# Kernel tuning notes

Measured on AMD Instinct MI355X. Metric: run time of the kernel, lower is better.

## Reference

```python
import jax, jax.numpy as jnp
import numpy as np

B, S, H, Q = 32, 128, 128, 3  # users, seq_len, hidden_size, quadkey_level
L = Q - 1  # number of mixing scales


def setup_inputs() -> dict:
    key = jax.random.key(0)
    ks = jax.random.split(key, 12)
    trend0 = jax.random.normal(ks[0], (B, S, H), dtype=jnp.float32)
    trend1 = jax.random.normal(ks[1], (B, S, H), dtype=jnp.float32)
    trend2 = jax.random.normal(ks[2], (B, S, H), dtype=jnp.float32)
    # Per-position prefix linears padded into dense tensors, zero-masked beyond
    # the prefix length j+1 so the ragged math is exact:
    #   W1[j, :j+1, :j+1] ~ Linear(j+1, j+1), b1[j, :j+1]
    #   W2[j, :j+1]      ~ Linear(j+1, 1),   b2[j]
    idx = jnp.arange(S)
    pm = (idx[None, :] <= idx[:, None]).astype(jnp.float32)  # [j, s]: s <= j
    W1 = jax.random.normal(ks[3], (L, S, S, S), dtype=jnp.float32) * 0.05
    W1 = W1 * pm[None, :, :, None] * pm[None, :, None, :]
    b1 = jax.random.normal(ks[4], (L, S, S), dtype=jnp.float32) * 0.05 * pm[None]
    W2 = jax.random.normal(ks[5], (L, S, S), dtype=jnp.float32) * 0.05 * pm[None]
    b2 = jax.random.normal(ks[6], (L, S), dtype=jnp.float32) * 0.05
    # shared output MLP: Linear(H,H)->GELU->Linear(H,H); stored as [in, out]
    Wm1 = jax.random.normal(ks[7], (H, H), dtype=jnp.float32) * 0.05
    bm1 = jax.random.normal(ks[8], (H,), dtype=jnp.float32) * 0.05
    Wm2 = jax.random.normal(ks[9], (H, H), dtype=jnp.float32) * 0.05
    bm2 = jax.random.normal(ks[10], (H,), dtype=jnp.float32) * 0.05
    return {"trend0": trend0, "trend1": trend1, "trend2": trend2,
            "W1": W1, "b1": b1, "W2": W2, "b2": b2,
            "Wm1": Wm1, "bm1": bm1, "Wm2": Wm2, "bm2": bm2}


def reference(trend0, trend1, trend2, W1, b1, W2, b2, Wm1, bm1, Wm2, bm2):
    gelu = lambda x: jax.nn.gelu(x, approximate=False)  # torch nn.GELU default
    mlp = lambda x: gelu(x @ Wm1 + bm1) @ Wm2 + bm2

    rev = [trend2, trend1, trend0]  # trend_list reversed
    out_low = rev[0]
    out_high = rev[1]
    outs = [out_low]
    for i in range(Q - 1):
        # vectorized ragged prefix mix: per position j, out_low[:, :j+1] (as [B,H,j+1])
        # -> Linear(j+1,j+1) -> GELU -> Linear(j+1,1). Zero-padding in W1/b1/W2
        # kills all contributions beyond the prefix (GELU(0)=0).
        y1 = jnp.einsum('bsh,jst->bhjt', out_low, W1[i]) + b1[i]  # [B,H,S,S]
        res = jnp.einsum('bhjt,jt->bjh', gelu(y1), W2[i]) + b2[i][None, :, None]
        out_high = out_high + res
        out_low = out_high
        if i + 2 <= Q - 1:
            out_high = rev[i + 2]
        out_low = mlp(out_low)
        outs.append(out_low)
    outs.reverse()
    return tuple(outs)
```

## Files before the change

kernel.cpp:

```cpp
#include <hip/hip_runtime.h>
#include <stdint.h>

#define BSH (32 * 128 * 128)

typedef __attribute__((ext_vector_type(8))) __bf16 bf16x8;
typedef __attribute__((ext_vector_type(4))) float f32x4;

__device__ __forceinline__ unsigned short f2bf(float f) {
  union { float f; unsigned u; } v; v.f = f;
  return (unsigned short)((v.u + 0x7FFFu + ((v.u >> 16) & 1u)) >> 16);
}

__device__ __forceinline__ float fast_exp2(float x) {
#if __has_builtin(__builtin_amdgcn_exp2f)
  return __builtin_amdgcn_exp2f(x);
#else
  float r; asm("v_exp_f32 %0, %1" : "=v"(r) : "v"(x)); return r;
#endif
}
__device__ __forceinline__ float fast_rcp(float x) {
#if __has_builtin(__builtin_amdgcn_rcpf)
  return __builtin_amdgcn_rcpf(x);
#else
  float r; asm("v_rcp_f32 %0, %1" : "=v"(r) : "v"(x)); return r;
#endif
}

__device__ __forceinline__ float gelu_f(float y) {
  float u = y * y;
  float p = __builtin_fmaf(u, 0.044715f, 1.0f) * y;
  float w = fast_exp2(p * 2.30220787f);
  return y - y * fast_rcp(1.0f + w);
}

__device__ __forceinline__ void transpose_part(const float* __restrict__ src,
                                               unsigned short* __restrict__ dst,
                                               unsigned short* lds, int part) {
  const int tid = threadIdx.x;
  const float4* s4 = (const float4*)(src) + part * 1024;
  __syncthreads();
#pragma unroll
  for (int it = 0; it < 4; ++it) {
    int i4 = tid + it * 256;
    float4 v = s4[i4];
    int s = i4 >> 5;
    int t0 = (i4 * 4) & 127;
    unsigned short t[4] __attribute__((aligned(8)));
    t[0] = f2bf(v.x); t[1] = f2bf(v.y); t[2] = f2bf(v.z); t[3] = f2bf(v.w);
    *(uint2*)(lds + s * 136 + t0) = *(const uint2*)t;
  }
  __syncthreads();
#pragma unroll
  for (int it = 0; it < 2; ++it) {
    int c = tid + it * 256;
    int kql = c >> 7, tr = c & 127;
    unsigned short tmp[8] __attribute__((aligned(16)));
#pragma unroll
    for (int e = 0; e < 8; ++e) tmp[e] = lds[(kql * 8 + e) * 136 + tr];
    *(uint4*)(dst + ((part * 4 + kql) * 128 + tr) * 8) = *(const uint4*)tmp;
  }
}

__global__ __launch_bounds__(256) void prepass_kernel(
    const float* __restrict__ W1, const float* __restrict__ trend2,
    const float* __restrict__ Wm1, const float* __restrict__ Wm2,
    unsigned short* __restrict__ W1Tc, unsigned short* __restrict__ T2c,
    unsigned short* __restrict__ Wm1c, unsigned short* __restrict__ Wm2c,
    float* __restrict__ out2) {
  __shared__ __align__(16) unsigned short lds[32 * 136];
  const int bid = blockIdx.x;
  if (bid < 1024) {
    int part = bid >> 8, w = bid & 255;
    int x = w & 7, i = w >> 3;
    int stage = i >> 4, u = i & 15;
    int m = u & 7, half = u >> 3;
    int jpp = x + 8 * m;
    int j = half ? 127 - jpp : jpp;
    int blk = stage * 128 + j;
    transpose_part(W1 + blk * 16384, W1Tc + blk * 16384, lds, part);
  } else if (bid < 1152) {
    int t = bid - 1024;
    int part = t >> 5, b = t & 31;
    transpose_part(trend2 + b * 16384, T2c + b * 16384, lds, part);
    const float4* s4 = (const float4*)(trend2 + b * 16384);
    float4* d4 = (float4*)(out2 + b * 16384);
#pragma unroll
    for (int it = 0; it < 4; ++it) {
      int i = part * 1024 + threadIdx.x + it * 256;
      d4[i] = s4[i];
    }
  } else if (bid == 1152) {
#pragma unroll
    for (int part = 0; part < 4; ++part)
      transpose_part(Wm1, Wm1c, lds, part);
  } else {
#pragma unroll
    for (int part = 0; part < 4; ++part)
      transpose_part(Wm2, Wm2c, lds, part);
  }
}

__global__ __launch_bounds__(256, 3) void mix_mlp_kernel(
    const unsigned short* __restrict__ XTc,
    const unsigned short* __restrict__ W1Tj,
    const float* __restrict__ b1j,
    const float* __restrict__ W2j,
    const float* __restrict__ b2j,
    const float* __restrict__ trendR,
    const unsigned short* __restrict__ Wm1c,
    const unsigned short* __restrict__ Wm2c,
    const float* __restrict__ bm1,
    const float* __restrict__ bm2,
    float* __restrict__ outA,
    unsigned short* __restrict__ outTc) {
  __shared__ float res[512];
  __shared__ __align__(16) float xrow[2][128];
  __shared__ __align__(16) unsigned short urow[2][128];
  const int bid = blockIdx.x;
  const int b = bid >> 6;
  const int jp = bid & 63;
  const int js = jp, jb = 127 - jp;
  const int tid = threadIdx.x;
  const int wave = tid >> 6;
  const int p = wave & 1;
  const int mh = wave >> 1;
  const int lane = tid & 63;
  const int lane15 = lane & 15;
  const int quad = lane >> 4;

  const int nt_s = (js >> 4) + 1;
  const int nt_b = (jb >> 4) + 1;

  const unsigned short* Bp = XTc + b * 16384 + (p * 64 + lane15) * 8;
  const unsigned short* As = W1Tj + js * 16384 + lane15 * 8;
  const unsigned short* Ab = W1Tj + jb * 16384 + lane15 * 8;
  const float C = -2.45546937f;

  bf16x8 Bv[4][4];
#pragma unroll
  for (int ks = 0; ks < 4; ++ks) {
    const int ko = (ks * 4 + quad) * 1024;
    Bv[ks][0] = *(const bf16x8*)(Bp + ko);
    Bv[ks][1] = *(const bf16x8*)(Bp + ko + 128);
    Bv[ks][2] = *(const bf16x8*)(Bp + ko + 256);
    Bv[ks][3] = *(const bf16x8*)(Bp + ko + 384);
  }

  float psum[2][4];
#pragma unroll
  for (int jj = 0; jj < 2; ++jj)
#pragma unroll
    for (int ni = 0; ni < 4; ++ni) psum[jj][ni] = 0.f;

  for (int mt = mh; mt < nt_b; mt += 2) {
    const int mo = mt * 128;
    bf16x8 a[4];
#pragma unroll
    for (int ks = 0; ks < 4; ++ks)
      a[ks] = *(const bf16x8*)(Ab + (ks * 4 + quad) * 1024 + mo);
    const int tb = mt * 16 + quad * 4;
    float4 b1v = *(const float4*)(b1j + jb * 128 + tb);
    float4 w2v = *(const float4*)(W2j + jb * 128 + tb);
    f32x4 acc[4];
#pragma unroll
    for (int ni = 0; ni < 4; ++ni) { f32x4 z = {0.f, 0.f, 0.f, 0.f}; acc[ni] = z; }
#pragma unroll
    for (int ks = 0; ks < 4; ++ks) {
      acc[0] = __builtin_amdgcn_mfma_f32_16x16x32_bf16(a[ks], Bv[ks][0], acc[0], 0, 0, 0);
      acc[1] = __builtin_amdgcn_mfma_f32_16x16x32_bf16(a[ks], Bv[ks][1], acc[1], 0, 0, 0);
      acc[2] = __builtin_amdgcn_mfma_f32_16x16x32_bf16(a[ks], Bv[ks][2], acc[2], 0, 0, 0);
      acc[3] = __builtin_amdgcn_mfma_f32_16x16x32_bf16(a[ks], Bv[ks][3], acc[3], 0, 0, 0);
    }
#pragma unroll
    for (int r = 0; r < 4; ++r) {
      float b1r = ((const float*)&b1v)[r];
      float w2r = ((const float*)&w2v)[r];
      float cb = C * b1r;
      float bw = b1r * w2r;
#pragma unroll
      for (int ni = 0; ni < 4; ++ni) {
        float av = acc[ni][r];
        float m = __builtin_fmaf(av, C, cb);
        float e = fast_exp2(m);
        float rr2 = fast_rcp(1.0f + e);
        float yw = __builtin_fmaf(av, w2r, bw);
        psum[1][ni] = __builtin_fmaf(yw, rr2, psum[1][ni]);
      }
    }
  }

  for (int mt = mh; mt < nt_s; mt += 2) {
    const int mo = mt * 128;
    bf16x8 a[2];
#pragma unroll
    for (int ks = 0; ks < 2; ++ks)
      a[ks] = *(const bf16x8*)(As + (ks * 4 + quad) * 1024 + mo);
    const int tb = mt * 16 + quad * 4;
    float4 b1v = *(const float4*)(b1j + js * 128 + tb);
    float4 w2v = *(const float4*)(W2j + js * 128 + tb);
    f32x4 acc[4];
#pragma unroll
    for (int ni = 0; ni < 4; ++ni) { f32x4 z = {0.f, 0.f, 0.f, 0.f}; acc[ni] = z; }
#pragma unroll
    for (int ks = 0; ks < 2; ++ks) {
      acc[0] = __builtin_amdgcn_mfma_f32_16x16x32_bf16(a[ks], Bv[ks][0], acc[0], 0, 0, 0);
      acc[1] = __builtin_amdgcn_mfma_f32_16x16x32_bf16(a[ks], Bv[ks][1], acc[1], 0, 0, 0);
      acc[2] = __builtin_amdgcn_mfma_f32_16x16x32_bf16(a[ks], Bv[ks][2], acc[2], 0, 0, 0);
      acc[3] = __builtin_amdgcn_mfma_f32_16x16x32_bf16(a[ks], Bv[ks][3], acc[3], 0, 0, 0);
    }
#pragma unroll
    for (int r = 0; r < 4; ++r) {
      float b1r = ((const float*)&b1v)[r];
      float w2r = ((const float*)&w2v)[r];
      float cb = C * b1r;
      float bw = b1r * w2r;
#pragma unroll
      for (int ni = 0; ni < 4; ++ni) {
        float av = acc[ni][r];
        float m = __builtin_fmaf(av, C, cb);
        float e = fast_exp2(m);
        float rr2 = fast_rcp(1.0f + e);
        float yw = __builtin_fmaf(av, w2r, bw);
        psum[0][ni] = __builtin_fmaf(yw, rr2, psum[0][ni]);
      }
    }
  }

#pragma unroll
  for (int jj = 0; jj < 2; ++jj)
#pragma unroll
    for (int ni = 0; ni < 4; ++ni) {
      float v = psum[jj][ni];
      v += __shfl_xor(v, 16, 64);
      v += __shfl_xor(v, 32, 64);
      psum[jj][ni] = v;
    }

  if (quad == 0) {
#pragma unroll
    for (int jj = 0; jj < 2; ++jj)
#pragma unroll
      for (int ni = 0; ni < 4; ++ni)
        res[wave * 128 + jj * 64 + ni * 16 + lane15] = psum[jj][ni];
  }
  __syncthreads();
  {
    const int l = tid & 15;
    const int nni = (tid >> 4) & 3;
    const int jj = (tid >> 6) & 1;
    const int pp = tid >> 7;
    const int j = jj ? jb : js;
    const int h = pp * 64 + nni * 16 + l;
    float v = res[tid] + res[tid + 256] + b2j[j] +
              trendR[(b * 128 + j) * 128 + h];
    xrow[jj][h] = v;
  }
  __syncthreads();

  const int arow = lane15 & 1;
  bf16x8 af[4];
#pragma unroll
  for (int ks = 0; ks < 4; ++ks) {
    const f32x4* xp = (const f32x4*)&xrow[arow][(ks * 4 + quad) * 8];
    f32x4 v0 = xp[0], v1 = xp[1];
    unsigned short t[8] __attribute__((aligned(16)));
    t[0] = f2bf(v0[0]); t[1] = f2bf(v0[1]); t[2] = f2bf(v0[2]); t[3] = f2bf(v0[3]);
    t[4] = f2bf(v1[0]); t[5] = f2bf(v1[1]); t[6] = f2bf(v1[2]); t[7] = f2bf(v1[3]);
    af[ks] = *(const bf16x8*)t;
  }
  f32x4 acc1[2];
  { f32x4 z = {0.f, 0.f, 0.f, 0.f}; acc1[0] = z; acc1[1] = z; }
#pragma unroll
  for (int ks = 0; ks < 4; ++ks) {
    int kq = ks * 4 + quad;
    bf16x8 w0 = *(const bf16x8*)(Wm1c + (kq * 128 + wave * 32 + lane15) * 8);
    bf16x8 w1 = *(const bf16x8*)(Wm1c + (kq * 128 + wave * 32 + 16 + lane15) * 8);
    acc1[0] = __builtin_amdgcn_mfma_f32_16x16x32_bf16(af[ks], w0, acc1[0], 0, 0, 0);
    acc1[1] = __builtin_amdgcn_mfma_f32_16x16x32_bf16(af[ks], w1, acc1[1], 0, 0, 0);
  }
  if (quad == 0) {
#pragma unroll
    for (int ni2 = 0; ni2 < 2; ++ni2) {
      int n = wave * 32 + ni2 * 16 + lane15;
      float bv = bm1[n];
      urow[0][n] = f2bf(gelu_f(acc1[ni2][0] + bv));
      urow[1][n] = f2bf(gelu_f(acc1[ni2][1] + bv));
    }
  }
  __syncthreads();
  bf16x8 uf[4];
#pragma unroll
  for (int ks = 0; ks < 4; ++ks)
    uf[ks] = *(const bf16x8*)&urow[arow][(ks * 4 + quad) * 8];
  f32x4 acc2[2];
  { f32x4 z = {0.f, 0.f, 0.f, 0.f}; acc2[0] = z; acc2[1] = z; }
#pragma unroll
  for (int ks = 0; ks < 4; ++ks) {
    int kq = ks * 4 + quad;
    bf16x8 w0 = *(const bf16x8*)(Wm2c + (kq * 128 + wave * 32 + lane15) * 8);
    bf16x8 w1 = *(const bf16x8*)(Wm2c + (kq * 128 + wave * 32 + 16 + lane15) * 8);
    acc2[0] = __builtin_amdgcn_mfma_f32_16x16x32_bf16(uf[ks], w0, acc2[0], 0, 0, 0);
    acc2[1] = __builtin_amdgcn_mfma_f32_16x16x32_bf16(uf[ks], w1, acc2[1], 0, 0, 0);
  }
  if (quad == 0) {
#pragma unroll
    for (int ni2 = 0; ni2 < 2; ++ni2) {
      int n = wave * 32 + ni2 * 16 + lane15;
      float bv = bm2[n];
#pragma unroll
      for (int r = 0; r < 2; ++r) {
        int j = r ? jb : js;
        float v = acc2[ni2][r] + bv;
        outA[(b * 128 + j) * 128 + n] = v;
        if (outTc)
          outTc[b * 16384 + ((j >> 3) * 128 + n) * 8 + (j & 7)] = f2bf(v);
      }
    }
  }
}

extern "C" void kernel_launch(void* const* d_in, const int* in_sizes, int n_in,
                              void* d_out, int out_size, void* d_ws, size_t ws_size,
                              hipStream_t stream) {
  (void)in_sizes; (void)n_in; (void)out_size; (void)ws_size;
  const float* trend0 = (const float*)d_in[0];
  const float* trend1 = (const float*)d_in[1];
  const float* trend2 = (const float*)d_in[2];
  const float* W1  = (const float*)d_in[3];
  const float* b1  = (const float*)d_in[4];
  const float* W2  = (const float*)d_in[5];
  const float* b2  = (const float*)d_in[6];
  const float* Wm1 = (const float*)d_in[7];
  const float* bm1 = (const float*)d_in[8];
  const float* Wm2 = (const float*)d_in[9];
  const float* bm2 = (const float*)d_in[10];
  float* out = (float*)d_out;
  char* ws = (char*)d_ws;

  unsigned short* W1Tc = (unsigned short*)(ws);
  unsigned short* T2c  = (unsigned short*)(ws + 8388608);
  unsigned short* A1Tc = (unsigned short*)(ws + 9437184);
  unsigned short* Wm1c = (unsigned short*)(ws + 10485760);
  unsigned short* Wm2c = (unsigned short*)(ws + 10518528);

  prepass_kernel<<<1154, 256, 0, stream>>>(W1, trend2, Wm1, Wm2,
                                           W1Tc, T2c, Wm1c, Wm2c, out + 2 * BSH);
  mix_mlp_kernel<<<2048, 256, 0, stream>>>(T2c, W1Tc, b1, W2, b2, trend1,
                                           Wm1c, Wm2c, bm1, bm2,
                                           out + BSH, A1Tc);
  mix_mlp_kernel<<<2048, 256, 0, stream>>>(A1Tc, W1Tc + 128 * 16384, b1 + 16384,
                                           W2 + 16384, b2 + 128, trend0,
                                           Wm1c, Wm2c, bm1, bm2,
                                           out, (unsigned short*)nullptr);
}
```

Measured before the change: 139.9 us.

## Process four position pairs per block to amortize activation loads and MLP

Each mix_mlp block now handles four (j, 127-j) position pairs instead of one, so the bf16 activation fragments loaded into registers are reused across four pairs. The MLP stage then runs on 8 rows instead of 2, so the MFMA tiles are better filled. The grid shrinks from 2048 to 512 blocks. The prepass also remaps which W1 slices each block transposes so they line up with the new grouping. The trade-off is less parallelism, with 512 blocks on a large GPU, and longer serial loops per block, which can cause load imbalance.

```diff
diff --git a/kernel.cpp b/kernel.cpp
--- a/kernel.cpp
+++ b/kernel.cpp
@@ -74,7 +74,7 @@
     int x = w & 7, i = w >> 3;
     int stage = i >> 4, u = i & 15;
     int m = u & 7, half = u >> 3;
-    int jpp = x + 8 * m;
+    int jpp = 4 * x + (m & 3) + 32 * (m >> 2);
     int j = half ? 127 - jpp : jpp;
     int blk = stage * 128 + j;
     transpose_part(W1 + blk * 16384, W1Tc + blk * 16384, lds, part);
@@ -113,13 +113,12 @@
     const float* __restrict__ bm2,
     float* __restrict__ outA,
     unsigned short* __restrict__ outTc) {
-  __shared__ float res[512];
-  __shared__ __align__(16) float xrow[2][128];
-  __shared__ __align__(16) unsigned short urow[2][128];
+  __shared__ float res[4 * 512];
+  __shared__ __align__(16) float xrow[8][128];
+  __shared__ __align__(16) unsigned short urow[8][128];
   const int bid = blockIdx.x;
-  const int b = bid >> 6;
-  const int jp = bid & 63;
-  const int js = jp, jb = 127 - jp;
+  const int b = bid >> 4;
+  const int jg = bid & 15;
   const int tid = threadIdx.x;
   const int wave = tid >> 6;
   const int p = wave & 1;
@@ -128,12 +127,7 @@
   const int lane15 = lane & 15;
   const int quad = lane >> 4;
 
-  const int nt_s = (js >> 4) + 1;
-  const int nt_b = (jb >> 4) + 1;
-
   const unsigned short* Bp = XTc + b * 16384 + (p * 64 + lane15) * 8;
-  const unsigned short* As = W1Tj + js * 16384 + lane15 * 8;
-  const unsigned short* Ab = W1Tj + jb * 16384 + lane15 * 8;
   const float C = -2.45546937f;
 
   bf16x8 Bv[4][4];
@@ -146,118 +140,131 @@
     Bv[ks][3] = *(const bf16x8*)(Bp + ko + 384);
   }
 
-  float psum[2][4];
-#pragma unroll
-  for (int jj = 0; jj < 2; ++jj)
-#pragma unroll
-    for (int ni = 0; ni < 4; ++ni) psum[jj][ni] = 0.f;
-
-  for (int mt = mh; mt < nt_b; mt += 2) {
-    const int mo = mt * 128;
-    bf16x8 a[4];
-#pragma unroll
-    for (int ks = 0; ks < 4; ++ks)
-      a[ks] = *(const bf16x8*)(Ab + (ks * 4 + quad) * 1024 + mo);
-    const int tb = mt * 16 + quad * 4;
-    float4 b1v = *(const float4*)(b1j + jb * 128 + tb);
-    float4 w2v = *(const float4*)(W2j + jb * 128 + tb);
-    f32x4 acc[4];
-#pragma unroll
-    for (int ni = 0; ni < 4; ++ni) { f32x4 z = {0.f, 0.f, 0.f, 0.f}; acc[ni] = z; }
-#pragma unroll
-    for (int ks = 0; ks < 4; ++ks) {
-      acc[0] = __builtin_amdgcn_mfma_f32_16x16x32_bf16(a[ks], Bv[ks][0], acc[0], 0, 0, 0);
-      acc[1] = __builtin_amdgcn_mfma_f32_16x16x32_bf16(a[ks], Bv[ks][1], acc[1], 0, 0, 0);
-      acc[2] = __builtin_amdgcn_mfma_f32_16x16x32_bf16(a[ks], Bv[ks][2], acc[2], 0, 0, 0);
-      acc[3] = __builtin_amdgcn_mfma_f32_16x16x32_bf16(a[ks], Bv[ks][3], acc[3], 0, 0, 0);
-    }
-#pragma unroll
-    for (int r = 0; r < 4; ++r) {
-      float b1r = ((const float*)&b1v)[r];
-      float w2r = ((const float*)&w2v)[r];
-      float cb = C * b1r;
-      float bw = b1r * w2r;
+  for (int g = 0; g < 4; ++g) {
+    const int jp = jg * 4 + g;
+    const int js = jp, jb = 127 - jp;
+    const int nt_s = (js >> 4) + 1;
+    const int nt_b = (jb >> 4) + 1;
+    const unsigned short* As = W1Tj + js * 16384 + lane15 * 8;
+    const unsigned short* Ab = W1Tj + jb * 16384 + lane15 * 8;
+
+    float psum[2][4];
+#pragma unroll
+    for (int jj = 0; jj < 2; ++jj)
+#pragma unroll
+      for (int ni = 0; ni < 4; ++ni) psum[jj][ni] = 0.f;
+
+    for (int mt = mh; mt < nt_b; mt += 2) {
+      const int mo = mt * 128;
+      bf16x8 a[4];
+#pragma unroll
+      for (int ks = 0; ks < 4; ++ks)
+        a[ks] = *(const bf16x8*)(Ab + (ks * 4 + quad) * 1024 + mo);
+      const int tb = mt * 16 + quad * 4;
+      float4 b1v = *(const float4*)(b1j + jb * 128 + tb);
+      float4 w2v = *(const float4*)(W2j + jb * 128 + tb);
+      f32x4 acc[4];
+#pragma unroll
+      for (int ni = 0; ni < 4; ++ni) { f32x4 z = {0.f, 0.f, 0.f, 0.f}; acc[ni] = z; }
+#pragma unroll
+      for (int ks = 0; ks < 4; ++ks) {
+        acc[0] = __builtin_amdgcn_mfma_f32_16x16x32_bf16(a[ks], Bv[ks][0], acc[0], 0, 0, 0);
+        acc[1] = __builtin_amdgcn_mfma_f32_16x16x32_bf16(a[ks], Bv[ks][1], acc[1], 0, 0, 0);
+        acc[2] = __builtin_amdgcn_mfma_f32_16x16x32_bf16(a[ks], Bv[ks][2], acc[2], 0, 0, 0);
+        acc[3] = __builtin_amdgcn_mfma_f32_16x16x32_bf16(a[ks], Bv[ks][3], acc[3], 0, 0, 0);
+      }
+#pragma unroll
+      for (int r = 0; r < 4; ++r) {
+        float b1r = ((const float*)&b1v)[r];
+        float w2r = ((const float*)&w2v)[r];
+        float cb = C * b1r;
+        float bw = b1r * w2r;
+#pragma unroll
+        for (int ni = 0; ni < 4; ++ni) {
+          float av = acc[ni][r];
+          float m = __builtin_fmaf(av, C, cb);
+          float e = fast_exp2(m);
+          float rr2 = fast_rcp(1.0f + e);
+          float yw = __builtin_fmaf(av, w2r, bw);
+          psum[1][ni] = __builtin_fmaf(yw, rr2, psum[1][ni]);
+        }
+      }
+    }
+
+    for (int mt = mh; mt < nt_s; mt += 2) {
+      const int mo = mt * 128;
+      bf16x8 a[2];
+#pragma unroll
+      for (int ks = 0; ks < 2; ++ks)
+        a[ks] = *(const bf16x8*)(As + (ks * 4 + quad) * 1024 + mo);
+      const int tb = mt * 16 + quad * 4;
+      float4 b1v = *(const float4*)(b1j + js * 128 + tb);
+      float4 w2v = *(const float4*)(W2j + js * 128 + tb);
+      f32x4 acc[4];
+#pragma unroll
+      for (int ni = 0; ni < 4; ++ni) { f32x4 z = {0.f, 0.f, 0.f, 0.f}; acc[ni] = z; }
+#pragma unroll
+      for (int ks = 0; ks < 2; ++ks) {
+        acc[0] = __builtin_amdgcn_mfma_f32_16x16x32_bf16(a[ks], Bv[ks][0], acc[0], 0, 0, 0);
+        acc[1] = __builtin_amdgcn_mfma_f32_16x16x32_bf16(a[ks], Bv[ks][1], acc[1], 0, 0, 0);
+        acc[2] = __builtin_amdgcn_mfma_f32_16x16x32_bf16(a[ks], Bv[ks][2], acc[2], 0, 0, 0);
+        acc[3] = __builtin_amdgcn_mfma_f32_16x16x32_bf16(a[ks], Bv[ks][3], acc[3], 0, 0, 0);
+      }
+#pragma unroll
+      for (int r = 0; r < 4; ++r) {
+        float b1r = ((const float*)&b1v)[r];
+        float w2r = ((const float*)&w2v)[r];
+        float cb = C * b1r;
+        float bw = b1r * w2r;
+#pragma unroll
+        for (int ni = 0; ni < 4; ++ni) {
+          float av = acc[ni][r];
+          float m = __builtin_fmaf(av, C, cb);
+          float e = fast_exp2(m);
+          float rr2 = fast_rcp(1.0f + e);
+          float yw = __builtin_fmaf(av, w2r, bw);
+          psum[0][ni] = __builtin_fmaf(yw, rr2, psum[0][ni]);
+        }
+      }
+    }
+
+#pragma unroll
+    for (int jj = 0; jj < 2; ++jj)
 #pragma unroll
       for (int ni = 0; ni < 4; ++ni) {
-        float av = acc[ni][r];
-        float m = __builtin_fmaf(av, C, cb);
-        float e = fast_exp2(m);
-        float rr2 = fast_rcp(1.0f + e);
-        float yw = __builtin_fmaf(av, w2r, bw);
-        psum[1][ni] = __builtin_fmaf(yw, rr2, psum[1][ni]);
-      }
-    }
-  }
-
-  for (int mt = mh; mt < nt_s; mt += 2) {
-    const int mo = mt * 128;
-    bf16x8 a[2];
-#pragma unroll
-    for (int ks = 0; ks < 2; ++ks)
-      a[ks] = *(const bf16x8*)(As + (ks * 4 + quad) * 1024 + mo);
-    const int tb = mt * 16 + quad * 4;
-    float4 b1v = *(const float4*)(b1j + js * 128 + tb);
-    float4 w2v = *(const float4*)(W2j + js * 128 + tb);
-    f32x4 acc[4];
-#pragma unroll
-    for (int ni = 0; ni < 4; ++ni) { f32x4 z = {0.f, 0.f, 0.f, 0.f}; acc[ni] = z; }
-#pragma unroll
-    for (int ks = 0; ks < 2; ++ks) {
-      acc[0] = __builtin_amdgcn_mfma_f32_16x16x32_bf16(a[ks], Bv[ks][0], acc[0], 0, 0, 0);
-      acc[1] = __builtin_amdgcn_mfma_f32_16x16x32_bf16(a[ks], Bv[ks][1], acc[1], 0, 0, 0);
-      acc[2] = __builtin_amdgcn_mfma_f32_16x16x32_bf16(a[ks], Bv[ks][2], acc[2], 0, 0, 0);
-      acc[3] = __builtin_amdgcn_mfma_f32_16x16x32_bf16(a[ks], Bv[ks][3], acc[3], 0, 0, 0);
-    }
-#pragma unroll
-    for (int r = 0; r < 4; ++r) {
-      float b1r = ((const float*)&b1v)[r];
-      float w2r = ((const float*)&w2v)[r];
-      float cb = C * b1r;
-      float bw = b1r * w2r;
-#pragma unroll
-      for (int ni = 0; ni < 4; ++ni) {
-        float av = acc[ni][r];
-        float m = __builtin_fmaf(av, C, cb);
-        float e = fast_exp2(m);
-        float rr2 = fast_rcp(1.0f + e);
-        float yw = __builtin_fmaf(av, w2r, bw);
-        psum[0][ni] = __builtin_fmaf(yw, rr2, psum[0][ni]);
-      }
-    }
-  }
-
-#pragma unroll
-  for (int jj = 0; jj < 2; ++jj)
-#pragma unroll
-    for (int ni = 0; ni < 4; ++ni) {
-      float v = psum[jj][ni];
-      v += __shfl_xor(v, 16, 64);
-      v += __shfl_xor(v, 32, 64);
-      psum[jj][ni] = v;
-    }
-
-  if (quad == 0) {
-#pragma unroll
-    for (int jj = 0; jj < 2; ++jj)
-#pragma unroll
-      for (int ni = 0; ni < 4; ++ni)
-        res[wave * 128 + jj * 64 + ni * 16 + lane15] = psum[jj][ni];
-  }
-  __syncthreads();
+        float v = psum[jj][ni];
+        v += __shfl_xor(v, 16, 64);
+        v += __shfl_xor(v, 32, 64);
+        psum[jj][ni] = v;
+      }
+    if (quad == 0) {
+#pragma unroll
+      for (int jj = 0; jj < 2; ++jj)
+#pragma unroll
+        for (int ni = 0; ni < 4; ++ni)
+          res[g * 512 + wave * 128 + jj * 64 + ni * 16 + lane15] = psum[jj][ni];
+    }
+  }
+  __syncthreads();
+
   {
     const int l = tid & 15;
     const int nni = (tid >> 4) & 3;
     const int jj = (tid >> 6) & 1;
     const int pp = tid >> 7;
-    const int j = jj ? jb : js;
     const int h = pp * 64 + nni * 16 + l;
-    float v = res[tid] + res[tid + 256] + b2j[j] +
-              trendR[(b * 128 + j) * 128 + h];
-    xrow[jj][h] = v;
-  }
-  __syncthreads();
-
-  const int arow = lane15 & 1;
+#pragma unroll
+    for (int g = 0; g < 4; ++g) {
+      const int jp = jg * 4 + g;
+      const int j = jj ? 127 - jp : jp;
+      float v = res[g * 512 + tid] + res[g * 512 + tid + 256] + b2j[j] +
+                trendR[(b * 128 + j) * 128 + h];
+      xrow[g * 2 + jj][h] = v;
+    }
+  }
+  __syncthreads();
+
+  const int arow = lane15 & 7;
   bf16x8 af[4];
 #pragma unroll
   for (int ks = 0; ks < 4; ++ks) {
@@ -278,13 +285,14 @@
     acc1[0] = __builtin_amdgcn_mfma_f32_16x16x32_bf16(af[ks], w0, acc1[0], 0, 0, 0);
     acc1[1] = __builtin_amdgcn_mfma_f32_16x16x32_bf16(af[ks], w1, acc1[1], 0, 0, 0);
   }
-  if (quad == 0) {
+  if (quad < 2) {
 #pragma unroll
     for (int ni2 = 0; ni2 < 2; ++ni2) {
       int n = wave * 32 + ni2 * 16 + lane15;
       float bv = bm1[n];
-      urow[0][n] = f2bf(gelu_f(acc1[ni2][0] + bv));
-      urow[1][n] = f2bf(gelu_f(acc1[ni2][1] + bv));
+#pragma unroll
+      for (int r = 0; r < 4; ++r)
+        urow[quad * 4 + r][n] = f2bf(gelu_f(acc1[ni2][r] + bv));
     }
   }
   __syncthreads();
@@ -302,14 +310,17 @@
     acc2[0] = __builtin_amdgcn_mfma_f32_16x16x32_bf16(uf[ks], w0, acc2[0], 0, 0, 0);
     acc2[1] = __builtin_amdgcn_mfma_f32_16x16x32_bf16(uf[ks], w1, acc2[1], 0, 0, 0);
   }
-  if (quad == 0) {
+  if (quad < 2) {
 #pragma unroll
     for (int ni2 = 0; ni2 < 2; ++ni2) {
       int n = wave * 32 + ni2 * 16 + lane15;
       float bv = bm2[n];
 #pragma unroll
-      for (int r = 0; r < 2; ++r) {
-        int j = r ? jb : js;
+      for (int r = 0; r < 4; ++r) {
+        int row8 = quad * 4 + r;
+        int g = row8 >> 1, jj = row8 & 1;
+        int jp = jg * 4 + g;
+        int j = jj ? 127 - jp : jp;
         float v = acc2[ni2][r] + bv;
         outA[(b * 128 + j) * 128 + n] = v;
         if (outTc)
@@ -345,11 +356,11 @@
 
   prepass_kernel<<<1154, 256, 0, stream>>>(W1, trend2, Wm1, Wm2,
                                            W1Tc, T2c, Wm1c, Wm2c, out + 2 * BSH);
-  mix_mlp_kernel<<<2048, 256, 0, stream>>>(T2c, W1Tc, b1, W2, b2, trend1,
-                                           Wm1c, Wm2c, bm1, bm2,
-                                           out + BSH, A1Tc);
-  mix_mlp_kernel<<<2048, 256, 0, stream>>>(A1Tc, W1Tc + 128 * 16384, b1 + 16384,
-                                           W2 + 16384, b2 + 128, trend0,
-                                           Wm1c, Wm2c, bm1, bm2,
-                                           out, (unsigned short*)nullptr);
-}
+  mix_mlp_kernel<<<512, 256, 0, stream>>>(T2c, W1Tc, b1, W2, b2, trend1,
+                                          Wm1c, Wm2c, bm1, bm2,
+                                          out + BSH, A1Tc);
+  mix_mlp_kernel<<<512, 256, 0, stream>>>(A1Tc, W1Tc + 128 * 16384, b1 + 16384,
+                                          W2 + 16384, b2 + 128, trend0,
+                                          Wm1c, Wm2c, bm1, bm2,
+                                          out, (unsigned short*)nullptr);
+}
```

After: 145.9 us. 1.04x slower.
